# Kernel optimization log

Hardware: AMD Instinct MI355X
Metric: run time of the kernel (lower is better)

## Reference

```python
import jax, jax.numpy as jnp
import numpy as np

B, S, D, H = 1, 2048, 1024, 16
DH = D // H  # 64
HID = 4 * D
EPS = 1e-5
NEG = -1.0e9


def setup_inputs() -> dict:
    key = jax.random.key(0)
    ks = jax.random.split(key, 12)
    s = 0.02
    return {
        "y": jax.random.normal(ks[0], (B, S, D), jnp.float32),
        "encoder_output": jax.random.normal(ks[1], (B, S, D), jnp.float32),
        # per-head shared projection (query_fc used for q,k,v — faithful to source bug)
        "Wq_self": jax.random.normal(ks[2], (H, D, DH), jnp.float32) * s,
        "bq_self": jax.random.normal(ks[3], (H, DH), jnp.float32) * s,
        "Wq_cross": jax.random.normal(ks[4], (H, D, DH), jnp.float32) * s,
        "bq_cross": jax.random.normal(ks[5], (H, DH), jnp.float32) * s,
        "g1": jnp.ones((D,), jnp.float32), "beta1": jnp.zeros((D,), jnp.float32),
        "g2": jnp.ones((D,), jnp.float32), "beta2": jnp.zeros((D,), jnp.float32),
        "g3": jnp.ones((D,), jnp.float32), "beta3": jnp.zeros((D,), jnp.float32),
        "w1": jax.random.normal(ks[6], (D, HID), jnp.float32) * s,
        "b1": jax.random.normal(ks[7], (HID,), jnp.float32) * s,
        "w2": jax.random.normal(ks[8], (HID, D), jnp.float32) * s,
        "b2": jax.random.normal(ks[9], (D,), jnp.float32) * s,
    }


def _layernorm(x, g, b):
    mu = jnp.mean(x, axis=-1, keepdims=True)
    var = jnp.mean((x - mu) ** 2, axis=-1, keepdims=True)
    return (x - mu) * jax.lax.rsqrt(var + EPS) * g + b


def _mha(x_q, x_kv, W, bias, causal):
    # source bug: q, k, v all use query_fc projection
    q = jnp.einsum('bsd,hde->bhse', x_q, W) + bias[None, :, None, :]
    k = jnp.einsum('bsd,hde->bhse', x_kv, W) + bias[None, :, None, :]
    v = jnp.einsum('bsd,hde->bhse', x_kv, W) + bias[None, :, None, :]
    scores = jnp.einsum('bhse,bhte->bhst', q, k) / jnp.sqrt(jnp.float32(DH))
    if causal:
        sq, sk = scores.shape[-2], scores.shape[-1]
        mask = jnp.triu(jnp.ones((sq, sk), bool), k=1)
        scores = jnp.where(mask, NEG, scores)
    p = jax.nn.softmax(scores, axis=-1)
    out = jnp.einsum('bhst,bhte->bhse', p, v)  # [B,H,S,DH]
    b, h, s, e = out.shape
    return out.transpose(0, 2, 1, 3).reshape(b, s, h * e)


def reference(y, encoder_output, Wq_self, bq_self, Wq_cross, bq_cross,
              g1, beta1, g2, beta2, g3, beta3, w1, b1, w2, b2):
    sa = _mha(y, y, Wq_self, bq_self, causal=True)
    y1 = _layernorm(y + sa, g1, beta1)
    ca = _mha(y1, encoder_output, Wq_cross, bq_cross, causal=False)
    y2 = _layernorm(y1 + ca, g2, beta2)
    ff = jnp.maximum(y2 @ w1 + b1, 0.0) @ w2 + b2
    return _layernorm(y2 + ff, g3, beta3)
```

## Files before the change

kernel.cpp:

```cpp
#include <hip/hip_runtime.h>
#include <hip/hip_bf16.h>


#define S_LEN 2048
#define DMODEL 1024
#define NHEAD 16
#define DHEAD 64
#define HIDDEN 4096

using bf16 = __hip_bfloat16;
typedef __attribute__((ext_vector_type(8))) short bf16x8;
typedef __attribute__((ext_vector_type(4))) float floatx4;

__device__ __forceinline__ void async_ld16(const void* g, void* l) {
  __builtin_amdgcn_global_load_lds(
      (const __attribute__((address_space(1))) unsigned int*)g,
      (__attribute__((address_space(3))) unsigned int*)l, 16, 0, 0);
}

__device__ __forceinline__ unsigned short f2bf_bits(float f) {
  __hip_bfloat16 b = __float2bfloat16(f);
  return *(unsigned short*)&b;
}

__device__ __forceinline__ unsigned int pk_bf16(float a, float b) {
  unsigned int r;
  asm("v_cvt_pk_bf16_f32 %0, %1, %2" : "=v"(r) : "v"(a), "v"(b));
  return r;
}

template <bool HEADB>
__global__ __launch_bounds__(256) void transp_bf16_kernel(
    const float* __restrict__ src0, bf16* __restrict__ dst0,
    const float* __restrict__ src1, bf16* __restrict__ dst1, int K, int N) {
  const float* src = blockIdx.z ? src1 : src0;
  bf16* dst = blockIdx.z ? dst1 : dst0;
  __shared__ float tile[32][33];
  const int tx = threadIdx.x & 31, ty = threadIdx.x >> 5;
  const int k0 = blockIdx.y * 32, n0 = blockIdx.x * 32;
#pragma unroll
  for (int i = 0; i < 4; ++i) {
    const int k = k0 + ty + i * 8;
    const int n = n0 + tx;
    size_t idx;
    if (HEADB)
      idx = (size_t)(n >> 6) * ((size_t)K * 64) + (size_t)k * 64 + (n & 63);
    else
      idx = (size_t)k * N + n;
    tile[ty + i * 8][tx] = src[idx];
  }
  __syncthreads();
#pragma unroll
  for (int i = 0; i < 4; ++i) {
    const int n = n0 + ty + i * 8;
    const int k = k0 + tx;
    dst[(size_t)n * K + k] = __float2bfloat16(tile[tx][ty + i * 8]);
  }
}

__global__ __launch_bounds__(256) void conv_bf16_kernel(
    const float* __restrict__ src0, bf16* __restrict__ dst0,
    const float* __restrict__ src1, bf16* __restrict__ dst1, int n4) {
  const float* src = blockIdx.z ? src1 : src0;
  bf16* dst = blockIdx.z ? dst1 : dst0;
  const int i = blockIdx.x * 256 + threadIdx.x;
  if (i >= n4) return;
  float4 v = ((const float4*)src)[i];
  ((uint2*)dst)[i] = make_uint2(pk_bf16(v.x, v.y), pk_bf16(v.z, v.w));
}

template <int BM, int BN, bool RELU, bool DUALT, typename CT>
__global__ __launch_bounds__(256) void mfma_gemm_kernel(
    const bf16* __restrict__ A0, const bf16* __restrict__ Bt0,
    const float* __restrict__ bias0, CT* __restrict__ C0,
    bf16* __restrict__ Ct0,
    const bf16* __restrict__ A1, const bf16* __restrict__ Bt1,
    const float* __restrict__ bias1, CT* __restrict__ C1,
    bf16* __restrict__ Ct1,
    int M, int N, int Kstride, int Klen) {
  const bf16* A = blockIdx.z ? A1 : A0;
  const bf16* Bt = blockIdx.z ? Bt1 : Bt0;
  const float* bias = blockIdx.z ? bias1 : bias0;
  CT* C = blockIdx.z ? C1 : C0;
  bf16* Ct = blockIdx.z ? Ct1 : Ct0;

  constexpr int MF = (BM + 31) / 32;
  constexpr int NF = BN / 32;
  __shared__ __align__(16) bf16 As[2][BM * 64];
  __shared__ __align__(16) bf16 Bs[2][BN * 64];

  const int tid = threadIdx.x;
  const int wave = tid >> 6;
  const int lane = tid & 63;
  const int m0 = blockIdx.y * BM;
  const int n0 = blockIdx.x * BN;
  const int wr = wave >> 1, wc = wave & 1;

  const int srow = tid >> 3;
  const int schunk = (tid & 7) ^ (srow & 7);
  const bf16* astg = A + (size_t)(m0 + srow) * Kstride + schunk * 8;
  const bf16* bstg = Bt + (size_t)(n0 + srow) * Kstride + schunk * 8;

  floatx4 acc[MF][NF];
#pragma unroll
  for (int i = 0; i < MF; ++i)
#pragma unroll
    for (int j = 0; j < NF; ++j) acc[i][j] = floatx4{0.f, 0.f, 0.f, 0.f};

  const int mrow = lane & 15;
  const int p0 = (((lane >> 4) ^ (mrow & 7)) << 4);
  const int p1 = p0 ^ 64;

  auto stage = [&](int buf) {
    char* al = (char*)As + buf * (BM * 128) + wave * 1024;
    char* bl = (char*)Bs + buf * (BN * 128) + wave * 1024;
#pragma unroll
    for (int i = 0; i < BM / 32; ++i)
      async_ld16(astg + (size_t)(32 * i) * Kstride, al + i * 4096);
#pragma unroll
    for (int i = 0; i < BN / 32; ++i)
      async_ld16(bstg + (size_t)(32 * i) * Kstride, bl + i * 4096);
  };

  stage(0);
  astg += 64;
  bstg += 64;
  __syncthreads();

  int cur = 0;
  for (int kt = 0; kt < Klen; kt += 64) {
    const char* abase = (const char*)As + cur * (BM * 128);
    const char* bbase = (const char*)Bs + cur * (BN * 128);
    bf16x8 af0[MF], af1[MF], bf0[NF], bf1[NF];
#pragma unroll
    for (int fi = 0; fi < MF; ++fi) {
      const char* ar = abase + (wr * (BM / 2) + fi * 16 + mrow) * 128;
      af0[fi] = *(const bf16x8*)(ar + p0);
      af1[fi] = *(const bf16x8*)(ar + p1);
    }
#pragma unroll
    for (int fj = 0; fj < NF; ++fj) {
      const char* br = bbase + (wc * (BN / 2) + fj * 16 + mrow) * 128;
      bf0[fj] = *(const bf16x8*)(br + p0);
      bf1[fj] = *(const bf16x8*)(br + p1);
    }

    if (kt + 64 < Klen) {
      stage(cur ^ 1);
      astg += 64;
      bstg += 64;
    }

#pragma unroll
    for (int fi = 0; fi < MF; ++fi)
#pragma unroll
      for (int fj = 0; fj < NF; ++fj) {
        acc[fi][fj] = __builtin_amdgcn_mfma_f32_16x16x32_bf16(
            af0[fi], bf0[fj], acc[fi][fj], 0, 0, 0);
        acc[fi][fj] = __builtin_amdgcn_mfma_f32_16x16x32_bf16(
            af1[fi], bf1[fj], acc[fi][fj], 0, 0, 0);
      }

    __syncthreads();
    cur ^= 1;
  }

  const int erow = (lane >> 4) * 4;
  const int ecol = lane & 15;
#pragma unroll
  for (int fi = 0; fi < MF; ++fi) {
#pragma unroll
    for (int fj = 0; fj < NF; ++fj) {
      const int nn = n0 + wc * (BN / 2) + fj * 16 + ecol;
      const float bv = bias ? bias[nn] : 0.0f;
      const int mmb = m0 + wr * (BM / 2) + fi * 16 + erow;
      float v[4];
#pragma unroll
      for (int r = 0; r < 4; ++r) {
        v[r] = acc[fi][fj][r] + bv;
        if (RELU) v[r] = fmaxf(v[r], 0.0f);
        if constexpr (sizeof(CT) == 2)
          C[(size_t)(mmb + r) * N + nn] = (CT)__float2bfloat16(v[r]);
        else
          C[(size_t)(mmb + r) * N + nn] = (CT)v[r];
      }
      if (DUALT) {
        *(uint2*)&Ct[(size_t)nn * M + mmb] =
            make_uint2(pk_bf16(v[0], v[1]), pk_bf16(v[2], v[3]));
      }
    }
  }
}

template <bool CAUSAL>
__global__ __launch_bounds__(256) void mfma_attn_kernel(
    const bf16* __restrict__ Q, const bf16* __restrict__ K,
    const bf16* __restrict__ Vt,
    float* __restrict__ OA, float* __restrict__ OB,
    float* __restrict__ LA, float* __restrict__ LB) {
  __shared__ __align__(16) unsigned short Kt[2][32 * 64];
  __shared__ __align__(16) unsigned short Vs[2][64 * 32];
  __shared__ __align__(16) unsigned short Ps[4][512];

  const int tid = threadIdx.x;
  const int w = tid >> 6, lane = tid & 63;
  const int g = lane >> 4, c = lane & 15;
  const int h = blockIdx.y;
  const int z = blockIdx.z;
  float* Oz = z ? OB : OA;
  float* Lz = z ? LB : LA;

  const int srk = tid >> 3;
  const int sck = (tid & 7) ^ (srk & 7);
  const bf16* kgp = K + (size_t)srk * DMODEL + h * DHEAD + sck * 8;
  const int srv = tid >> 2;
  const int scv = (tid & 3) ^ ((srv >> 1) & 3);
  const bf16* vgp = Vt + (size_t)(h * DHEAD + srv) * S_LEN + scv * 8;

  const int kpos0 = ((g ^ (c & 7)) << 4);
  const int kpos1 = kpos0 ^ 64;
  const int vpos = ((g ^ ((c >> 1) & 3)) << 4);
  char* pswave = (char*)Ps + w * 1024;

  const int ko00 = c * 128 + kpos0, ko01 = c * 128 + kpos1;
  const int ko10 = (16 + c) * 128 + kpos0, ko11 = (16 + c) * 128 + kpos1;
  const int vo0 = c * 64 + vpos, vo1 = (16 + c) * 64 + vpos;
  const int vo2 = (32 + c) * 64 + vpos, vo3 = (48 + c) * 64 + vpos;
  char* const pw0 = pswave + c * 64 +
      ((((g >> 1) ^ ((c >> 1) & 3)) << 4) | ((g & 1) << 3));
  char* const pw1 = pswave + c * 64 +
      ((((2 + (g >> 1)) ^ ((c >> 1) & 3)) << 4) | ((g & 1) << 3));
  const char* const pr = pswave + vo0;

  const int npass = CAUSAL ? 2 : 1;
  for (int pass = 0; pass < npass; ++pass) {
    const int qb = CAUSAL ? (pass ? (S_LEN / 64 - 1) - (int)blockIdx.x
                                  : (int)blockIdx.x)
                          : (int)blockIdx.x;
    const int q0 = qb * 64;
    const int qw = q0 + w * 16;

    const bf16* qrow = Q + (size_t)(qw + c) * DMODEL + h * DHEAD + g * 8;
    const bf16x8 qfa = *(const bf16x8*)qrow;
    const bf16x8 qfb = *(const bf16x8*)(qrow + 32);

    floatx4 of0{0.f, 0.f, 0.f, 0.f}, of1{0.f, 0.f, 0.f, 0.f};
    floatx4 of2{0.f, 0.f, 0.f, 0.f}, of3{0.f, 0.f, 0.f, 0.f};
    float lp0 = 0.f, lp1 = 0.f;

    const int nkt = CAUSAL ? (q0 / 32 + 2) : (S_LEN / 32);

    const bf16* kst = kgp + (size_t)(z * 32) * DMODEL;
    const bf16* vst = vgp + z * 32;

    auto phase = [&](const char* kb, const char* vb, int sbuf, int kt) {
      bool act = true;
      if constexpr (CAUSAL) act = !(kt * 32 >= qw + 16);
      bf16x8 kf00, kf01, kf10, kf11, vf0, vf1, vf2, vf3;
      if (act) {
        kf00 = *(const bf16x8*)(kb + ko00);
        kf01 = *(const bf16x8*)(kb + ko01);
        kf10 = *(const bf16x8*)(kb + ko10);
        kf11 = *(const bf16x8*)(kb + ko11);
        vf0 = *(const bf16x8*)(vb + vo0);
        vf1 = *(const bf16x8*)(vb + vo1);
        vf2 = *(const bf16x8*)(vb + vo2);
        vf3 = *(const bf16x8*)(vb + vo3);
      }
      if (kt + 2 < nkt) {
        async_ld16(kst, (char*)Kt + sbuf * 4096 + w * 1024);
        async_ld16(vst, (char*)Vs + sbuf * 4096 + w * 1024);
        kst += (size_t)64 * DMODEL;
        vst += 64;
      }
      if (act) {
#pragma unroll
        for (int jt = 0; jt < 2; ++jt) {
          floatx4 s = floatx4{0.f, 0.f, 0.f, 0.f};
          __builtin_amdgcn_s_setprio(1);
          s = __builtin_amdgcn_mfma_f32_16x16x32_bf16(jt ? kf10 : kf00, qfa, s, 0, 0, 0);
          s = __builtin_amdgcn_mfma_f32_16x16x32_bf16(jt ? kf11 : kf01, qfb, s, 0, 0, 0);
          __builtin_amdgcn_s_setprio(0);

          const float C = 0.18033688011f;
          float e0, e1, e2, e3;
          {
            float x0 = s[0] * C, x1 = s[1] * C, x2 = s[2] * C, x3 = s[3] * C;
            asm("v_exp_f32 %0, %1" : "=v"(e0) : "v"(x0));
            asm("v_exp_f32 %0, %1" : "=v"(e1) : "v"(x1));
            asm("v_exp_f32 %0, %1" : "=v"(e2) : "v"(x2));
            asm("v_exp_f32 %0, %1" : "=v"(e3) : "v"(x3));
          }
          if constexpr (CAUSAL) {
            const bool diag = (kt * 32 + 32 > qw);
            if (diag) {
              const int tb = kt * 32 + 16 * jt + 4 * g;
              const int qq = qw + c;
              if (tb + 0 > qq) e0 = 0.f;
              if (tb + 1 > qq) e1 = 0.f;
              if (tb + 2 > qq) e2 = 0.f;
              if (tb + 3 > qq) e3 = 0.f;
            }
          }
          lp0 += e0 + e1;
          lp1 += e2 + e3;
          *(uint2*)(jt ? pw1 : pw0) =
              make_uint2(pk_bf16(e0, e1), pk_bf16(e2, e3));
        }

        const bf16x8 pf = *(const bf16x8*)pr;
        __builtin_amdgcn_s_setprio(1);
        of0 = __builtin_amdgcn_mfma_f32_16x16x32_bf16(vf0, pf, of0, 0, 0, 0);
        of1 = __builtin_amdgcn_mfma_f32_16x16x32_bf16(vf1, pf, of1, 0, 0, 0);
        of2 = __builtin_amdgcn_mfma_f32_16x16x32_bf16(vf2, pf, of2, 0, 0, 0);
        of3 = __builtin_amdgcn_mfma_f32_16x16x32_bf16(vf3, pf, of3, 0, 0, 0);
        __builtin_amdgcn_s_setprio(0);
      }
      __syncthreads();
    };

    async_ld16(kst, (char*)Kt + w * 1024);
    async_ld16(vst, (char*)Vs + w * 1024);
    kst += (size_t)64 * DMODEL;
    vst += 64;
    __syncthreads();

    int kt = z;
    while (true) {
      phase((const char*)Kt, (const char*)Vs, 1, kt);
      kt += 2;
      if (kt >= nkt) break;
      phase((const char*)Kt + 4096, (const char*)Vs + 4096, 0, kt);
      kt += 2;
      if (kt >= nkt) break;
    }

    float lpart = lp0 + lp1;
    lpart += __shfl_xor(lpart, 16, 64);
    lpart += __shfl_xor(lpart, 32, 64);
    if (g == 0) Lz[(size_t)h * S_LEN + qw + c] = lpart;
    float* orow = Oz + (size_t)(qw + c) * DMODEL + h * DHEAD;
    {
      float4 v;
      v.x = of0[0]; v.y = of0[1]; v.z = of0[2]; v.w = of0[3];
      *(float4*)(orow + 0 * 16 + 4 * g) = v;
      v.x = of1[0]; v.y = of1[1]; v.z = of1[2]; v.w = of1[3];
      *(float4*)(orow + 1 * 16 + 4 * g) = v;
      v.x = of2[0]; v.y = of2[1]; v.z = of2[2]; v.w = of2[3];
      *(float4*)(orow + 2 * 16 + 4 * g) = v;
      v.x = of3[0]; v.y = of3[1]; v.z = of3[2]; v.w = of3[3];
      *(float4*)(orow + 3 * 16 + 4 * g) = v;
    }
  }
}

template <bool DUAL, bool MERGE, bool SUM2>
__global__ __launch_bounds__(256) void add_ln_kernel(
    const float* __restrict__ X, const float* __restrict__ R,
    const float* __restrict__ R2, const float* __restrict__ bvec,
    const float* __restrict__ La, const float* __restrict__ Lb,
    const float* __restrict__ g, const float* __restrict__ beta,
    float* __restrict__ out, bf16* __restrict__ out2) {
  const int row = blockIdx.x;
  const int tid = threadIdx.x;
  const int c = tid * 4;
  const size_t base = (size_t)row * DMODEL + c;

  float4 x = *(const float4*)&X[base];
  if (MERGE) {
    const int h = c >> 6;
    const float rl =
        1.0f / (La[(size_t)h * S_LEN + row] + Lb[(size_t)h * S_LEN + row]);
    const float4 r = *(const float4*)&R[base];
    const float4 r2 = *(const float4*)&R2[base];
    x.x += (r.x + r2.x) * rl;
    x.y += (r.y + r2.y) * rl;
    x.z += (r.z + r2.z) * rl;
    x.w += (r.w + r2.w) * rl;
  } else if (SUM2) {
    const float4 r = *(const float4*)&R[base];
    const float4 r2 = *(const float4*)&R2[base];
    const float4 bv = *(const float4*)&bvec[c];
    x.x += r.x + r2.x + bv.x;
    x.y += r.y + r2.y + bv.y;
    x.z += r.z + r2.z + bv.z;
    x.w += r.w + r2.w + bv.w;
  } else {
    const float4 r = *(const float4*)&R[base];
    x.x += r.x; x.y += r.y; x.z += r.z; x.w += r.w;
  }
  float s1 = x.x + x.y + x.z + x.w;
  float s2 = x.x * x.x + x.y * x.y + x.z * x.z + x.w * x.w;

#pragma unroll
  for (int off = 32; off; off >>= 1) {
    s1 += __shfl_xor(s1, off, 64);
    s2 += __shfl_xor(s2, off, 64);
  }
  __shared__ float w1s[4], w2s[4];
  const int wid = tid >> 6, lane = tid & 63;
  if (lane == 0) { w1s[wid] = s1; w2s[wid] = s2; }
  __syncthreads();
  s1 = w1s[0] + w1s[1] + w1s[2] + w1s[3];
  s2 = w2s[0] + w2s[1] + w2s[2] + w2s[3];

  const float mu = s1 * (1.0f / DMODEL);
  const float var = s2 * (1.0f / DMODEL) - mu * mu;
  const float rstd = rsqrtf(var + 1e-5f);

  const float4 gg = *(const float4*)&g[c];
  const float4 bb = *(const float4*)&beta[c];
  float4 r;
  r.x = (x.x - mu) * rstd * gg.x + bb.x;
  r.y = (x.y - mu) * rstd * gg.y + bb.y;
  r.z = (x.z - mu) * rstd * gg.z + bb.z;
  r.w = (x.w - mu) * rstd * gg.w + bb.w;
  *(float4*)&out[base] = r;
  if (DUAL) {
    *(uint2*)&out2[base] = make_uint2(pk_bf16(r.x, r.y), pk_bf16(r.z, r.w));
  }
}

extern "C" void kernel_launch(void* const* d_in, const int* in_sizes, int n_in,
                              void* d_out, int out_size, void* d_ws, size_t ws_size,
                              hipStream_t stream) {
  const float* y      = (const float*)d_in[0];
  const float* enc    = (const float*)d_in[1];
  const float* Wself  = (const float*)d_in[2];
  const float* bself  = (const float*)d_in[3];
  const float* Wcross = (const float*)d_in[4];
  const float* bcross = (const float*)d_in[5];
  const float* g1     = (const float*)d_in[6];
  const float* be1    = (const float*)d_in[7];
  const float* g2     = (const float*)d_in[8];
  const float* be2    = (const float*)d_in[9];
  const float* g3     = (const float*)d_in[10];
  const float* be3    = (const float*)d_in[11];
  const float* w1     = (const float*)d_in[12];
  const float* b1     = (const float*)d_in[13];
  const float* w2     = (const float*)d_in[14];
  const float* b2     = (const float*)d_in[15];
  float* out = (float*)d_out;

  char* ws = (char*)d_ws;
  const size_t MB = 1024 * 1024;
  bf16*  ybf   = (bf16*)(ws + 0 * MB);
  bf16*  encbf = (bf16*)(ws + 4 * MB);
  float* PA    = (float*)(ws + 0 * MB);
  float* PB    = (float*)(ws + 8 * MB);
  float* Y1    = (float*)(ws + 16 * MB);
  float* Y2    = (float*)(ws + 24 * MB);
  bf16*  Q12b  = (bf16*)(ws + 32 * MB);
  bf16*  Q1t   = (bf16*)(ws + 36 * MB);
  bf16*  K2b   = (bf16*)(ws + 40 * MB);
  bf16*  K2t   = (bf16*)(ws + 44 * MB);
  bf16*  w1t   = (bf16*)(ws + 48 * MB);
  bf16*  w2t   = (bf16*)(ws + 56 * MB);
  bf16*  Wst   = (bf16*)(ws + 64 * MB);
  bf16*  Wct   = (bf16*)(ws + 66 * MB);
  bf16*  Y1bf  = (bf16*)(ws + 68 * MB);
  bf16*  Y2bf  = (bf16*)(ws + 72 * MB);
  float* La    = (float*)(ws + 76 * MB);
  float* Lb    = (float*)(ws + 76 * MB + 512 * 1024);
  bf16*  FFH   = (bf16*)(ws + 0 * MB);
  float* FFa   = (float*)(ws + 32 * MB);
  float* FFb   = (float*)(ws + 40 * MB);

  const dim3 blk(256);
  const dim3 gT_w(DMODEL / 32, DMODEL / 32, 2);
  const dim3 gT_w1(HIDDEN / 32, DMODEL / 32);
  const dim3 gT_w2(DMODEL / 32, HIDDEN / 32);
  const dim3 gConv(S_LEN * DMODEL / 4 / 256, 1, 2);
  const dim3 gProj2(DMODEL / 64, S_LEN / 128, 2);
  const dim3 gProj(DMODEL / 64, S_LEN / 64);
  const dim3 gFf1(HIDDEN / 128, S_LEN / 128);
  const dim3 gFf2(DMODEL / 64, S_LEN / 128, 2);
  const dim3 gAttnC(S_LEN / 128, NHEAD, 2);
  const dim3 gAttnX(S_LEN / 64, NHEAD, 2);
  const dim3 gLn(S_LEN);

  transp_bf16_kernel<true><<<gT_w, blk, 0, stream>>>(
      Wself, Wst, Wcross, Wct, DMODEL, DMODEL);
  transp_bf16_kernel<false><<<gT_w1, blk, 0, stream>>>(
      w1, w1t, nullptr, nullptr, DMODEL, HIDDEN);
  transp_bf16_kernel<false><<<gT_w2, blk, 0, stream>>>(
      w2, w2t, nullptr, nullptr, HIDDEN, DMODEL);
  conv_bf16_kernel<<<gConv, blk, 0, stream>>>(
      y, ybf, enc, encbf, S_LEN * DMODEL / 4);

  mfma_gemm_kernel<128, 64, false, true, bf16><<<gProj2, blk, 0, stream>>>(
      ybf, Wst, bself, Q12b, Q1t,
      encbf, Wct, bcross, K2b, K2t, S_LEN, DMODEL, DMODEL, DMODEL);
  mfma_attn_kernel<true><<<gAttnC, blk, 0, stream>>>(
      Q12b, Q12b, Q1t, PA, PB, La, Lb);
  add_ln_kernel<true, true, false><<<gLn, blk, 0, stream>>>(
      y, PA, PB, nullptr, La, Lb, g1, be1, Y1, Y1bf);
  mfma_gemm_kernel<64, 64, false, false, bf16><<<gProj, blk, 0, stream>>>(
      Y1bf, Wct, bcross, Q12b, nullptr,
      nullptr, nullptr, nullptr, nullptr, nullptr, S_LEN, DMODEL, DMODEL, DMODEL);
  mfma_attn_kernel<false><<<gAttnX, blk, 0, stream>>>(
      Q12b, K2b, K2t, PA, PB, La, Lb);
  add_ln_kernel<true, true, false><<<gLn, blk, 0, stream>>>(
      Y1, PA, PB, nullptr, La, Lb, g2, be2, Y2, Y2bf);
  mfma_gemm_kernel<128, 128, true, false, bf16><<<gFf1, blk, 0, stream>>>(
      Y2bf, w1t, b1, FFH, nullptr,
      nullptr, nullptr, nullptr, nullptr, nullptr, S_LEN, HIDDEN, DMODEL, DMODEL);
  mfma_gemm_kernel<128, 64, false, false, float><<<gFf2, blk, 0, stream>>>(
      FFH, w2t, nullptr, FFa, nullptr,
      FFH + HIDDEN / 2, w2t + HIDDEN / 2, nullptr, FFb, nullptr,
      S_LEN, DMODEL, HIDDEN, HIDDEN / 2);
  add_ln_kernel<false, false, true><<<gLn, blk, 0, stream>>>(
      Y2, FFa, FFb, b2, nullptr, nullptr, g3, be3, out, nullptr);
}
```

Measured before the change: 291.6 us.

## Widen attention key tiles to 64 and fuse weight/input conversion kernels

The attention kernel now processes 64 keys per tile instead of 32, with a doubled LDS staging buffer and two MFMAs per PV accumulation. The aim is to halve the number of barrier-synchronised phases and amortise the fixed cost of each. Separately, the four transpose and convert launches are merged into one kernel that dispatches on block index, saving launch overhead. The trade-off is more LDS per block, which may lower occupancy, and more wasted masked work on diagonal tiles in the causal case.

```diff
diff --git a/kernel.cpp b/kernel.cpp
--- a/kernel.cpp
+++ b/kernel.cpp
@@ -30,14 +30,11 @@
 }
 
 template <bool HEADB>
-__global__ __launch_bounds__(256) void transp_bf16_kernel(
-    const float* __restrict__ src0, bf16* __restrict__ dst0,
-    const float* __restrict__ src1, bf16* __restrict__ dst1, int K, int N) {
-  const float* src = blockIdx.z ? src1 : src0;
-  bf16* dst = blockIdx.z ? dst1 : dst0;
-  __shared__ float tile[32][33];
+__device__ __forceinline__ void transp_body(
+    const float* __restrict__ src, bf16* __restrict__ dst, int K, int N,
+    int bx, int by, float (*tile)[33]) {
   const int tx = threadIdx.x & 31, ty = threadIdx.x >> 5;
-  const int k0 = blockIdx.y * 32, n0 = blockIdx.x * 32;
+  const int k0 = by * 32, n0 = bx * 32;
 #pragma unroll
   for (int i = 0; i < 4; ++i) {
     const int k = k0 + ty + i * 8;
@@ -58,15 +55,33 @@
   }
 }
 
-__global__ __launch_bounds__(256) void conv_bf16_kernel(
-    const float* __restrict__ src0, bf16* __restrict__ dst0,
-    const float* __restrict__ src1, bf16* __restrict__ dst1, int n4) {
-  const float* src = blockIdx.z ? src1 : src0;
-  bf16* dst = blockIdx.z ? dst1 : dst0;
-  const int i = blockIdx.x * 256 + threadIdx.x;
-  if (i >= n4) return;
-  float4 v = ((const float4*)src)[i];
-  ((uint2*)dst)[i] = make_uint2(pk_bf16(v.x, v.y), pk_bf16(v.z, v.w));
+__global__ __launch_bounds__(256) void fused_conv_kernel(
+    const float* __restrict__ Wself, bf16* __restrict__ Wst,
+    const float* __restrict__ Wcross, bf16* __restrict__ Wct,
+    const float* __restrict__ w1, bf16* __restrict__ w1t,
+    const float* __restrict__ w2, bf16* __restrict__ w2t,
+    const float* __restrict__ y, bf16* __restrict__ ybf,
+    const float* __restrict__ enc, bf16* __restrict__ encbf) {
+  __shared__ float tile[32][33];
+  const int id = blockIdx.x;
+  if (id < 2048) {
+    const int p = id >> 10, r = id & 1023;
+    transp_body<true>(p ? Wcross : Wself, p ? Wct : Wst, DMODEL, DMODEL,
+                      r & 31, r >> 5, tile);
+  } else if (id < 6144) {
+    const int r = id - 2048;
+    transp_body<false>(w1, w1t, DMODEL, HIDDEN, r & 127, r >> 7, tile);
+  } else if (id < 10240) {
+    const int r = id - 6144;
+    transp_body<false>(w2, w2t, HIDDEN, DMODEL, r & 31, r >> 5, tile);
+  } else {
+    const int r = id - 10240;
+    const float* src = (r >> 11) ? enc : y;
+    bf16* dst = (r >> 11) ? encbf : ybf;
+    const int i = (r & 2047) * 256 + threadIdx.x;
+    float4 v = ((const float4*)src)[i];
+    ((uint2*)dst)[i] = make_uint2(pk_bf16(v.x, v.y), pk_bf16(v.z, v.w));
+  }
 }
 
 template <int BM, int BN, bool RELU, bool DUALT, typename CT>
@@ -198,9 +213,9 @@
     const bf16* __restrict__ Vt,
     float* __restrict__ OA, float* __restrict__ OB,
     float* __restrict__ LA, float* __restrict__ LB) {
-  __shared__ __align__(16) unsigned short Kt[2][32 * 64];
-  __shared__ __align__(16) unsigned short Vs[2][64 * 32];
-  __shared__ __align__(16) unsigned short Ps[4][512];
+  __shared__ __align__(16) unsigned short Kt[2][64 * 64];
+  __shared__ __align__(16) unsigned short Vs[2][64 * 64];
+  __shared__ __align__(16) unsigned short Ps[4][1024];
 
   const int tid = threadIdx.x;
   const int w = tid >> 6, lane = tid & 63;
@@ -210,27 +225,28 @@
   float* Oz = z ? OB : OA;
   float* Lz = z ? LB : LA;
 
-  const int srk = tid >> 3;
-  const int sck = (tid & 7) ^ (srk & 7);
-  const bf16* kgp = K + (size_t)srk * DMODEL + h * DHEAD + sck * 8;
-  const int srv = tid >> 2;
-  const int scv = (tid & 3) ^ ((srv >> 1) & 3);
-  const bf16* vgp = Vt + (size_t)(h * DHEAD + srv) * S_LEN + scv * 8;
-
-  const int kpos0 = ((g ^ (c & 7)) << 4);
-  const int kpos1 = kpos0 ^ 64;
-  const int vpos = ((g ^ ((c >> 1) & 3)) << 4);
-  char* pswave = (char*)Ps + w * 1024;
-
-  const int ko00 = c * 128 + kpos0, ko01 = c * 128 + kpos1;
-  const int ko10 = (16 + c) * 128 + kpos0, ko11 = (16 + c) * 128 + kpos1;
-  const int vo0 = c * 64 + vpos, vo1 = (16 + c) * 64 + vpos;
-  const int vo2 = (32 + c) * 64 + vpos, vo3 = (48 + c) * 64 + vpos;
-  char* const pw0 = pswave + c * 64 +
-      ((((g >> 1) ^ ((c >> 1) & 3)) << 4) | ((g & 1) << 3));
-  char* const pw1 = pswave + c * 64 +
-      ((((2 + (g >> 1)) ^ ((c >> 1) & 3)) << 4) | ((g & 1) << 3));
-  const char* const pr = pswave + vo0;
+  const int srow = tid >> 3;
+  const int schk = (tid & 7) ^ (srow & 7);
+  const bf16* kgp = K + (size_t)srow * DMODEL + h * DHEAD + schk * 8;
+  const bf16* vgp = Vt + (size_t)(h * DHEAD + srow) * S_LEN + schk * 8;
+
+  char* pswave = (char*)Ps + w * 2048;
+
+  int ko[4][2], vo[4][2];
+#pragma unroll
+  for (int i = 0; i < 4; ++i) {
+    ko[i][0] = (16 * i + c) * 128 + (((g) ^ (c & 7)) << 4);
+    ko[i][1] = (16 * i + c) * 128 + (((4 + g) ^ (c & 7)) << 4);
+    vo[i][0] = ko[i][0];
+    vo[i][1] = ko[i][1];
+  }
+  char* pw[4];
+#pragma unroll
+  for (int jt = 0; jt < 4; ++jt)
+    pw[jt] = pswave + c * 128 +
+             ((((2 * jt + (g >> 1)) ^ (c & 7)) << 4) | ((g & 1) << 3));
+  const char* const pr0 = pswave + c * 128 + (((g) ^ (c & 7)) << 4);
+  const char* const pr1 = pswave + c * 128 + (((4 + g) ^ (c & 7)) << 4);
 
   const int npass = CAUSAL ? 2 : 1;
   for (int pass = 0; pass < npass; ++pass) {
@@ -244,58 +260,66 @@
     const bf16x8 qfa = *(const bf16x8*)qrow;
     const bf16x8 qfb = *(const bf16x8*)(qrow + 32);
 
-    floatx4 of0{0.f, 0.f, 0.f, 0.f}, of1{0.f, 0.f, 0.f, 0.f};
-    floatx4 of2{0.f, 0.f, 0.f, 0.f}, of3{0.f, 0.f, 0.f, 0.f};
+    floatx4 of[4];
+#pragma unroll
+    for (int i = 0; i < 4; ++i) of[i] = floatx4{0.f, 0.f, 0.f, 0.f};
     float lp0 = 0.f, lp1 = 0.f;
 
-    const int nkt = CAUSAL ? (q0 / 32 + 2) : (S_LEN / 32);
-
-    const bf16* kst = kgp + (size_t)(z * 32) * DMODEL;
-    const bf16* vst = vgp + z * 32;
+    const int nkt = CAUSAL ? (qb + 1) : (S_LEN / 64);
+
+    const bf16* kst = kgp + (size_t)(z * 64) * DMODEL;
+    const bf16* vst = vgp + z * 64;
+
+    auto stage = [&](int buf) {
+      char* kl = (char*)Kt + buf * 8192 + w * 1024;
+      char* vl = (char*)Vs + buf * 8192 + w * 1024;
+      async_ld16(kst, kl);
+      async_ld16(kst + (size_t)32 * DMODEL, kl + 4096);
+      async_ld16(vst, vl);
+      async_ld16(vst + (size_t)32 * S_LEN, vl + 4096);
+      kst += (size_t)128 * DMODEL;
+      vst += 128;
+    };
 
     auto phase = [&](const char* kb, const char* vb, int sbuf, int kt) {
+      const int t0 = kt * 64;
       bool act = true;
-      if constexpr (CAUSAL) act = !(kt * 32 >= qw + 16);
-      bf16x8 kf00, kf01, kf10, kf11, vf0, vf1, vf2, vf3;
+      if constexpr (CAUSAL) act = (t0 < qw + 16);
+      bf16x8 vf[4][2];
       if (act) {
-        kf00 = *(const bf16x8*)(kb + ko00);
-        kf01 = *(const bf16x8*)(kb + ko01);
-        kf10 = *(const bf16x8*)(kb + ko10);
-        kf11 = *(const bf16x8*)(kb + ko11);
-        vf0 = *(const bf16x8*)(vb + vo0);
-        vf1 = *(const bf16x8*)(vb + vo1);
-        vf2 = *(const bf16x8*)(vb + vo2);
-        vf3 = *(const bf16x8*)(vb + vo3);
+#pragma unroll
+        for (int md = 0; md < 4; ++md) {
+          vf[md][0] = *(const bf16x8*)(vb + vo[md][0]);
+          vf[md][1] = *(const bf16x8*)(vb + vo[md][1]);
+        }
       }
-      if (kt + 2 < nkt) {
-        async_ld16(kst, (char*)Kt + sbuf * 4096 + w * 1024);
-        async_ld16(vst, (char*)Vs + sbuf * 4096 + w * 1024);
-        kst += (size_t)64 * DMODEL;
-        vst += 64;
-      }
+      if (kt + 2 < nkt) stage(sbuf);
       if (act) {
-#pragma unroll
-        for (int jt = 0; jt < 2; ++jt) {
+        const bool diag = CAUSAL && (t0 + 64 > qw);
+        const int qq = qw + c;
+#pragma unroll
+        for (int jt = 0; jt < 4; ++jt) {
+          const bf16x8 kf0 = *(const bf16x8*)(kb + ko[jt][0]);
+          const bf16x8 kf1 = *(const bf16x8*)(kb + ko[jt][1]);
           floatx4 s = floatx4{0.f, 0.f, 0.f, 0.f};
           __builtin_amdgcn_s_setprio(1);
-          s = __builtin_amdgcn_mfma_f32_16x16x32_bf16(jt ? kf10 : kf00, qfa, s, 0, 0, 0);
-          s = __builtin_amdgcn_mfma_f32_16x16x32_bf16(jt ? kf11 : kf01, qfb, s, 0, 0, 0);
+          s = __builtin_amdgcn_mfma_f32_16x16x32_bf16(kf0, qfa, s, 0, 0, 0);
+          s = __builtin_amdgcn_mfma_f32_16x16x32_bf16(kf1, qfb, s, 0, 0, 0);
           __builtin_amdgcn_s_setprio(0);
 
-          const float C = 0.18033688011f;
+          const float CC = 0.18033688011f;
           float e0, e1, e2, e3;
           {
-            float x0 = s[0] * C, x1 = s[1] * C, x2 = s[2] * C, x3 = s[3] * C;
+            float x0 = s[0] * CC, x1 = s[1] * CC;
+            float x2 = s[2] * CC, x3 = s[3] * CC;
             asm("v_exp_f32 %0, %1" : "=v"(e0) : "v"(x0));
             asm("v_exp_f32 %0, %1" : "=v"(e1) : "v"(x1));
             asm("v_exp_f32 %0, %1" : "=v"(e2) : "v"(x2));
             asm("v_exp_f32 %0, %1" : "=v"(e3) : "v"(x3));
           }
           if constexpr (CAUSAL) {
-            const bool diag = (kt * 32 + 32 > qw);
             if (diag) {
-              const int tb = kt * 32 + 16 * jt + 4 * g;
-              const int qq = qw + c;
+              const int tb = t0 + 16 * jt + 4 * g;
               if (tb + 0 > qq) e0 = 0.f;
               if (tb + 1 > qq) e1 = 0.f;
               if (tb + 2 > qq) e2 = 0.f;
@@ -304,25 +328,25 @@
           }
           lp0 += e0 + e1;
           lp1 += e2 + e3;
-          *(uint2*)(jt ? pw1 : pw0) =
-              make_uint2(pk_bf16(e0, e1), pk_bf16(e2, e3));
+          *(uint2*)pw[jt] = make_uint2(pk_bf16(e0, e1), pk_bf16(e2, e3));
         }
 
-        const bf16x8 pf = *(const bf16x8*)pr;
+        const bf16x8 pf0 = *(const bf16x8*)pr0;
+        const bf16x8 pf1 = *(const bf16x8*)pr1;
         __builtin_amdgcn_s_setprio(1);
-        of0 = __builtin_amdgcn_mfma_f32_16x16x32_bf16(vf0, pf, of0, 0, 0, 0);
-        of1 = __builtin_amdgcn_mfma_f32_16x16x32_bf16(vf1, pf, of1, 0, 0, 0);
-        of2 = __builtin_amdgcn_mfma_f32_16x16x32_bf16(vf2, pf, of2, 0, 0, 0);
-        of3 = __builtin_amdgcn_mfma_f32_16x16x32_bf16(vf3, pf, of3, 0, 0, 0);
+#pragma unroll
+        for (int md = 0; md < 4; ++md) {
+          of[md] = __builtin_amdgcn_mfma_f32_16x16x32_bf16(
+              vf[md][0], pf0, of[md], 0, 0, 0);
+          of[md] = __builtin_amdgcn_mfma_f32_16x16x32_bf16(
+              vf[md][1], pf1, of[md], 0, 0, 0);
+        }
         __builtin_amdgcn_s_setprio(0);
       }
       __syncthreads();
     };
 
-    async_ld16(kst, (char*)Kt + w * 1024);
-    async_ld16(vst, (char*)Vs + w * 1024);
-    kst += (size_t)64 * DMODEL;
-    vst += 64;
+    stage(0);
     __syncthreads();
 
     int kt = z;
@@ -330,7 +354,7 @@
       phase((const char*)Kt, (const char*)Vs, 1, kt);
       kt += 2;
       if (kt >= nkt) break;
-      phase((const char*)Kt + 4096, (const char*)Vs + 4096, 0, kt);
+      phase((const char*)Kt + 8192, (const char*)Vs + 8192, 0, kt);
       kt += 2;
       if (kt >= nkt) break;
     }
@@ -340,16 +364,11 @@
     lpart += __shfl_xor(lpart, 32, 64);
     if (g == 0) Lz[(size_t)h * S_LEN + qw + c] = lpart;
     float* orow = Oz + (size_t)(qw + c) * DMODEL + h * DHEAD;
-    {
+#pragma unroll
+    for (int md = 0; md < 4; ++md) {
       float4 v;
-      v.x = of0[0]; v.y = of0[1]; v.z = of0[2]; v.w = of0[3];
-      *(float4*)(orow + 0 * 16 + 4 * g) = v;
-      v.x = of1[0]; v.y = of1[1]; v.z = of1[2]; v.w = of1[3];
-      *(float4*)(orow + 1 * 16 + 4 * g) = v;
-      v.x = of2[0]; v.y = of2[1]; v.z = of2[2]; v.w = of2[3];
-      *(float4*)(orow + 2 * 16 + 4 * g) = v;
-      v.x = of3[0]; v.y = of3[1]; v.z = of3[2]; v.w = of3[3];
-      *(float4*)(orow + 3 * 16 + 4 * g) = v;
+      v.x = of[md][0]; v.y = of[md][1]; v.z = of[md][2]; v.w = of[md][3];
+      *(float4*)(orow + md * 16 + 4 * g) = v;
     }
   }
 }
@@ -467,10 +486,7 @@
   float* FFb   = (float*)(ws + 40 * MB);
 
   const dim3 blk(256);
-  const dim3 gT_w(DMODEL / 32, DMODEL / 32, 2);
-  const dim3 gT_w1(HIDDEN / 32, DMODEL / 32);
-  const dim3 gT_w2(DMODEL / 32, HIDDEN / 32);
-  const dim3 gConv(S_LEN * DMODEL / 4 / 256, 1, 2);
+  const dim3 gFused(14336);
   const dim3 gProj2(DMODEL / 64, S_LEN / 128, 2);
   const dim3 gProj(DMODEL / 64, S_LEN / 64);
   const dim3 gFf1(HIDDEN / 128, S_LEN / 128);
@@ -479,14 +495,8 @@
   const dim3 gAttnX(S_LEN / 64, NHEAD, 2);
   const dim3 gLn(S_LEN);
 
-  transp_bf16_kernel<true><<<gT_w, blk, 0, stream>>>(
-      Wself, Wst, Wcross, Wct, DMODEL, DMODEL);
-  transp_bf16_kernel<false><<<gT_w1, blk, 0, stream>>>(
-      w1, w1t, nullptr, nullptr, DMODEL, HIDDEN);
-  transp_bf16_kernel<false><<<gT_w2, blk, 0, stream>>>(
-      w2, w2t, nullptr, nullptr, HIDDEN, DMODEL);
-  conv_bf16_kernel<<<gConv, blk, 0, stream>>>(
-      y, ybf, enc, encbf, S_LEN * DMODEL / 4);
+  fused_conv_kernel<<<gFused, blk, 0, stream>>>(
+      Wself, Wst, Wcross, Wct, w1, w1t, w2, w2t, y, ybf, enc, encbf);
 
   mfma_gemm_kernel<128, 64, false, true, bf16><<<gProj2, blk, 0, stream>>>(
       ybf, Wst, bself, Q12b, Q1t,
```

Result: faster. 279.6 us (-4.1%).
